# Optimization experiments

Measured on AMD Instinct MI355X. Metric: run time of the kernel, lower is better.

The kernel has to match this reference:

```python
import jax, jax.numpy as jnp
import numpy as np


def mesa_head(xh, yh, qh, lam):
    # xh = per-head 'inputs' (v_proj output), yh = 'targets' (k_proj output),
    # qh = queries; all [T, d]. lam is this head's scalar lambda.
    T, d = xh.shape
    init_inv = jnp.eye(d, dtype=xh.dtype) * lam

    def step(inv, tok):
        x_t, q_t = tok
        Hx = inv @ x_t                      # [d]   (cur_inverse @ x)
        xH = x_t @ inv                      # [d]   (x^T @ cur_inverse)
        denom = 1.0 + x_t @ Hx              # scalar: forward=1 + x^T H x
        new_inv = inv - jnp.outer(Hx, xH) / denom   # Sherman-Morrison rank-1 update
        return new_inv, new_inv @ q_t       # pred_t = S_t @ q_t

    _, preds = jax.lax.scan(step, init_inv, (xh, qh))  # preds: [T, d]

    # scaled_dot_product_attention(preds, xh, yh) with masked=True,
    # use_softmax=False, normalization=False: tril-masked linear attention.
    logits = preds @ xh.T                               # [T, T]
    mask = jnp.tril(jnp.ones((T, T), dtype=bool))
    logits = jnp.where(mask, logits, jnp.zeros((), dtype=logits.dtype))
    return logits @ yh                                  # [T, d]


def reference(x, Wq, Wk, Wv, Wo, lambdas):
    B, T, E = x.shape
    H = lambdas.shape[0]
    d = Wq.shape[1] // H
    q = (x @ Wq).reshape(B, T, H, d)   # query_heads
    k = (x @ Wk).reshape(B, T, H, d)   # target_heads
    v = (x @ Wv).reshape(B, T, H, d)   # input_heads
    # Original call: mesa(input_heads, target_heads, query_heads, lambdas, norm)
    over_batch = jax.vmap(mesa_head, in_axes=(0, 0, 0, None))
    over_heads = jax.vmap(over_batch, in_axes=(2, 2, 2, 0), out_axes=-1)
    mesa_out = over_heads(v, k, q, lambdas)             # [B, T, d, H]
    # Faithful to original: reshape combines (d, H) in that order before o_proj.
    out = mesa_out.reshape(B, T, H * d) @ Wo            # [B, T, E]
    return out


def setup_inputs() -> dict:
    key = jax.random.key(0)
    ks = jax.random.split(key, 6)
    B, T, E, H, d = 2, 1024, 512, 8, 64
    s_in = 1.0 / np.sqrt(E).astype(np.float32)
    s_out = 1.0 / np.sqrt(H * d).astype(np.float32)
    return {
        "x": jax.random.normal(ks[0], (B, T, E), dtype=jnp.float32),
        "Wq": jax.random.normal(ks[1], (E, H * d), dtype=jnp.float32) * s_in,
        "Wk": jax.random.normal(ks[2], (E, H * d), dtype=jnp.float32) * s_in,
        "Wv": jax.random.normal(ks[3], (E, H * d), dtype=jnp.float32) * s_in,
        "Wo": jax.random.normal(ks[4], (H * d, E), dtype=jnp.float32) * s_out,
        "lambdas": jnp.ones((H,), dtype=jnp.float32),
    }
```

## Files before the change

### kernel.cpp

```cpp
#include <hip/hip_runtime.h>

#define T_SEQ 1024
#define DH 64
#define NH 8
#define NB 2
#define EMB 512
#define CS 32
#define NCH 32
#define ACH 16
#define NCHAIN 16

typedef __attribute__((ext_vector_type(8))) short bf16x8;
typedef __attribute__((ext_vector_type(4))) float f32x4;

__device__ __forceinline__ int swz4(int r, int c4) {
    return r * 16 + ((c4 ^ (r >> 2)) & 15);
}

__device__ __forceinline__ void fma4(float4& o, float s, const float4& b) {
    o.x += s * b.x; o.y += s * b.y; o.z += s * b.z; o.w += s * b.w;
}

__device__ __forceinline__ ushort f2bf(float f) {
    unsigned u = __float_as_uint(f);
    return (ushort)((u + 0x7FFFu + ((u >> 16) & 1u)) >> 16);
}
__device__ __forceinline__ float bf2f(ushort h) {
    return __uint_as_float(((unsigned)h) << 16);
}
__device__ __forceinline__ void split2(float f, ushort& hi, ushort& lo) {
    hi = f2bf(f);
    lo = f2bf(f - bf2f(hi));
}

__global__ __launch_bounds__(256) void prep_qkv(
    const float* __restrict__ x, const float* __restrict__ W0,
    const float* __restrict__ W1, const float* __restrict__ W2,
    ushort* __restrict__ x_hi, ushort* __restrict__ x_lo,
    ushort* __restrict__ Wt_hi, ushort* __restrict__ Wt_lo) {
    int zz = blockIdx.z;
    int t = threadIdx.x;
    __shared__ float T[64][65];
    if (zz < 3) {
        const float* W = (zz == 0) ? W0 : (zz == 1) ? W1 : W2;
        ushort* hi = Wt_hi + (size_t)zz * 262144;
        ushort* lo = Wt_lo + (size_t)zz * 262144;
        int kk0 = blockIdx.x * 64, n0 = blockIdx.y * 64;
#pragma unroll
        for (int i = 0; i < 4; ++i) {
            int rl = i * 16 + (t >> 4);
            float4 vv = *(const float4*)&W[(size_t)(kk0 + rl) * 512 + n0 + (t & 15) * 4];
            T[rl][(t & 15) * 4 + 0] = vv.x;
            T[rl][(t & 15) * 4 + 1] = vv.y;
            T[rl][(t & 15) * 4 + 2] = vv.z;
            T[rl][(t & 15) * 4 + 3] = vv.w;
        }
        __syncthreads();
        int nl = t >> 2, kl = (t & 3) * 16;
#pragma unroll
        for (int j4 = 0; j4 < 4; ++j4) {
            ushort4 h4, l4;
            split2(T[kl + j4 * 4 + 0][nl], h4.x, l4.x);
            split2(T[kl + j4 * 4 + 1][nl], h4.y, l4.y);
            split2(T[kl + j4 * 4 + 2][nl], h4.z, l4.z);
            split2(T[kl + j4 * 4 + 3][nl], h4.w, l4.w);
            size_t dst = (size_t)(n0 + nl) * 512 + kk0 + kl + j4 * 4;
            *(ushort4*)&hi[dst] = h4;
            *(ushort4*)&lo[dst] = l4;
        }
    } else {
        int bid = blockIdx.y * 8 + blockIdx.x;
        const float4* in = (const float4*)x;
        ushort4* hi = (ushort4*)x_hi;
        ushort4* lo = (ushort4*)x_lo;
#pragma unroll
        for (int i = 0; i < 16; ++i) {
            int id = (bid * 16 + i) * 256 + t;
            float4 xv = in[id];
            ushort4 h, l;
            split2(xv.x, h.x, l.x);
            split2(xv.y, h.y, l.y);
            split2(xv.z, h.z, l.z);
            split2(xv.w, h.w, l.w);
            hi[id] = h;
            lo[id] = l;
        }
    }
}

template <int MODE>
__global__ __launch_bounds__(256) void mfma_gemm(
    const ushort* __restrict__ Ahi, const ushort* __restrict__ Alo,
    const ushort* __restrict__ Bth, const ushort* __restrict__ Btl,
    float* __restrict__ o0, float* __restrict__ o1, float* __restrict__ o2) {
    int bm = blockIdx.x, bn = blockIdx.y, zz = blockIdx.z;
    const ushort* Bh = Bth + (size_t)zz * 262144;
    const ushort* Bl = Btl + (size_t)zz * 262144;
    float* out = (MODE == 0) ? ((zz == 0) ? o0 : (zz == 1) ? o1 : o2) : o0;

    __shared__ ushort Ash[128 * 40];
    __shared__ ushort Asl[128 * 40];
    __shared__ ushort Bsh[64 * 40];
    __shared__ ushort Bsl[64 * 40];

    int tid = threadIdx.x;
    int lane = tid & 63, wid = tid >> 6;
    int wm = wid >> 1, wn = wid & 1;
    int fr = lane & 15, fk = (lane >> 4) * 8;
    int sr = tid >> 2, sc = (tid & 3) * 8;

    f32x4 zero = {0.f, 0.f, 0.f, 0.f};
    f32x4 acc[4][2];
#pragma unroll
    for (int f = 0; f < 4; ++f)
#pragma unroll
        for (int g = 0; g < 2; ++g) acc[f][g] = zero;

    const ushort* gAh = Ahi + (size_t)(bm * 128 + sr) * 512 + sc;
    const ushort* gAl = Alo + (size_t)(bm * 128 + sr) * 512 + sc;
    const ushort* gBh = Bh + (size_t)(bn * 64 + sr) * 512 + sc;
    const ushort* gBl = Bl + (size_t)(bn * 64 + sr) * 512 + sc;

    for (int k0 = 0; k0 < 512; k0 += 32) {
        uint4 a0 = *(const uint4*)(gAh + k0);
        uint4 a1 = *(const uint4*)(gAh + 64 * 512 + k0);
        uint4 a2 = *(const uint4*)(gAl + k0);
        uint4 a3 = *(const uint4*)(gAl + 64 * 512 + k0);
        uint4 b0 = *(const uint4*)(gBh + k0);
        uint4 b1 = *(const uint4*)(gBl + k0);
        __syncthreads();
        *(uint4*)&Ash[sr * 40 + sc] = a0;
        *(uint4*)&Ash[(sr + 64) * 40 + sc] = a1;
        *(uint4*)&Asl[sr * 40 + sc] = a2;
        *(uint4*)&Asl[(sr + 64) * 40 + sc] = a3;
        *(uint4*)&Bsh[sr * 40 + sc] = b0;
        *(uint4*)&Bsl[sr * 40 + sc] = b1;
        __syncthreads();
        bf16x8 ah[4], al[4], bh[2], blo[2];
#pragma unroll
        for (int f = 0; f < 4; ++f) {
            int r = wm * 64 + f * 16 + fr;
            ah[f] = *(const bf16x8*)&Ash[r * 40 + fk];
            al[f] = *(const bf16x8*)&Asl[r * 40 + fk];
        }
#pragma unroll
        for (int g = 0; g < 2; ++g) {
            int r = wn * 32 + g * 16 + fr;
            bh[g] = *(const bf16x8*)&Bsh[r * 40 + fk];
            blo[g] = *(const bf16x8*)&Bsl[r * 40 + fk];
        }
#pragma unroll
        for (int f = 0; f < 4; ++f)
#pragma unroll
            for (int g = 0; g < 2; ++g) {
                acc[f][g] = __builtin_amdgcn_mfma_f32_16x16x32_bf16(
                    ah[f], bh[g], acc[f][g], 0, 0, 0);
                acc[f][g] = __builtin_amdgcn_mfma_f32_16x16x32_bf16(
                    ah[f], blo[g], acc[f][g], 0, 0, 0);
                acc[f][g] = __builtin_amdgcn_mfma_f32_16x16x32_bf16(
                    al[f], bh[g], acc[f][g], 0, 0, 0);
            }
    }

    int rbase = (lane >> 4) * 4;
#pragma unroll
    for (int f = 0; f < 4; ++f)
#pragma unroll
        for (int g = 0; g < 2; ++g)
#pragma unroll
            for (int j = 0; j < 4; ++j) {
                int m = bm * 128 + wm * 64 + f * 16 + rbase + j;
                int n = bn * 64 + wn * 32 + g * 16 + (lane & 15);
                float val = acc[f][g][j];
                if (MODE == 0) {
                    int b = m >> 10, tt = m & 1023;
                    int h = n >> 6, d = n & 63;
                    out[(((size_t)(b * 8 + h) * 1024 + tt) << 6) + d] = val;
                } else {
                    out[(size_t)m * 512 + n] = val;
                }
            }
}

__global__ __launch_bounds__(256) void gram_kernel(
    const float* __restrict__ v, float* __restrict__ g) {
    int chain = blockIdx.x, chunk = blockIdx.y;
    const float* X = v + ((size_t)chain * T_SEQ + chunk * CS) * DH;
    __shared__ float Xs[CS * 64];
    int tid = threadIdx.x;
#pragma unroll
    for (int i = 0; i < (CS * 16) / 256; ++i)
        ((float4*)Xs)[i * 256 + tid] = ((const float4*)X)[i * 256 + tid];
    __syncthreads();

    int tx = tid & 15, ty = tid >> 4;
    float acc[4][4];
#pragma unroll
    for (int i = 0; i < 4; ++i)
#pragma unroll
        for (int j = 0; j < 4; ++j) acc[i][j] = 0.f;

#pragma unroll 4
    for (int t = 0; t < CS; ++t) {
        float a_[4], b_[4];
#pragma unroll
        for (int i = 0; i < 4; ++i) a_[i] = Xs[t * 64 + ty * 4 + i];
#pragma unroll
        for (int j = 0; j < 4; ++j) b_[j] = Xs[t * 64 + tx * 4 + j];
#pragma unroll
        for (int i = 0; i < 4; ++i)
#pragma unroll
            for (int j = 0; j < 4; ++j) acc[i][j] += a_[i] * b_[j];
    }

    float* gp = g + ((size_t)chain * NCH + chunk) * 4096;
#pragma unroll
    for (int i = 0; i < 4; ++i)
        *(float4*)(gp + (ty * 4 + i) * 64 + tx * 4) =
            make_float4(acc[i][0], acc[i][1], acc[i][2], acc[i][3]);
}

__global__ __launch_bounds__(256) void prefix_kernel(float* __restrict__ g) {
    int gid = blockIdx.x * 256 + threadIdx.x;
    int chain = gid >> 12, elem = gid & 4095;
    float* p = g + (size_t)chain * NCH * 4096 + elem;
    float vals[NCH];
#pragma unroll
    for (int c = 0; c < NCH; ++c) vals[c] = p[(size_t)c * 4096];
    float run = 0.f;
#pragma unroll
    for (int c = 0; c < NCH; ++c) {
        float t = vals[c];
        vals[c] = run;
        run += t;
    }
#pragma unroll
    for (int c = 0; c < NCH; ++c) p[(size_t)c * 4096] = vals[c];
}

__global__ __launch_bounds__(256) void invscan_kv(
    int nInv,
    const float* __restrict__ g, const float* __restrict__ v,
    const float* __restrict__ q, const float* __restrict__ lambdas,
    float* __restrict__ preds,
    const float* __restrict__ Kv, float* __restrict__ D) {
    __shared__ float smem[8192];
    int bid = blockIdx.x;
    int tid = threadIdx.x;

    if (bid < nInv) {
        int chain = bid >> 5, chunk = bid & 31;
        int row = tid >> 2, ch = tid & 3, wav = tid >> 6;
        float lam = lambdas[chain & (NH - 1)];

        float* Xs = smem;
        float* Qs = smem + 2048;
        float* Po = smem + 4096;
        float* rbufB = smem + 6144;
        float* sbufB = smem + 6272;
        float* red = smem + 6400;

        float m[16];
        {
            const float4* gp = (const float4*)(g + ((size_t)chain * NCH + chunk) * 4096);
#pragma unroll
            for (int i = 0; i < 4; ++i) {
                float4 t4 = gp[row * 16 + ch * 4 + i];
                m[i * 4 + 0] = t4.x; m[i * 4 + 1] = t4.y;
                m[i * 4 + 2] = t4.z; m[i * 4 + 3] = t4.w;
            }
        }
#pragma unroll
        for (int i = 0; i < 16; ++i)
            if (ch * 16 + i == row) m[i] += lam;

        const float4* vb = (const float4*)(v + ((size_t)chain * T_SEQ + chunk * CS) * DH);
        const float4* qb = (const float4*)(q + ((size_t)chain * T_SEQ + chunk * CS) * DH);
        ((float4*)Xs)[tid] = vb[tid];
        ((float4*)Xs)[256 + tid] = vb[256 + tid];
        ((float4*)Qs)[tid] = qb[tid];
        ((float4*)Qs)[256 + tid] = qb[256 + tid];

        if (row == 0) {
#pragma unroll
            for (int i = 0; i < 4; ++i)
                ((float4*)rbufB)[ch * 4 + i] =
                    make_float4(m[i * 4], m[i * 4 + 1], m[i * 4 + 2], m[i * 4 + 3]);
        }
        if (row == 1) {
#pragma unroll
            for (int i = 0; i < 4; ++i)
                ((float4*)sbufB)[ch * 4 + i] =
                    make_float4(m[i * 4], m[i * 4 + 1], m[i * 4 + 2], m[i * 4 + 3]);
        }
        __syncthreads();

#pragma unroll
        for (int pp = 0; pp < 32; ++pp) {
            const int p = 2 * pp;
            const float* rb = rbufB + (pp & 1) * 64;
            const float* sb = sbufB + (pp & 1) * 64;
            float r_[16], s_[16];
#pragma unroll
            for (int i = 0; i < 4; ++i) {
                float4 t4 = ((const float4*)rb)[ch * 4 + i];
                r_[i * 4] = t4.x; r_[i * 4 + 1] = t4.y;
                r_[i * 4 + 2] = t4.z; r_[i * 4 + 3] = t4.w;
                float4 u4 = ((const float4*)sb)[ch * 4 + i];
                s_[i * 4] = u4.x; s_[i * 4 + 1] = u4.y;
                s_[i * 4 + 2] = u4.z; s_[i * 4 + 3] = u4.w;
            }
            float rp = rb[p], rp2 = rb[p + 1], sp2 = sb[p + 1];
            float gr = rb[row], gs = sb[row];
            float i1 = 1.f / rp;
            float al = rp2 * i1;
            float i2 = 1.f / (sp2 - al * rp2);
            float c0, ca, cb;
            if (row == p) {
                c0 = 0.f; ca = i1 + al * al * i2; cb = -al * i2;
            } else if (row == p + 1) {
                c0 = 0.f; ca = -al * i2; cb = i2;
            } else {
                float b2 = (gs - al * gr) * i2;
                c0 = 1.f; ca = al * b2 - gr * i1; cb = -b2;
            }
#pragma unroll
            for (int i = 0; i < 16; ++i) m[i] = c0 * m[i] + ca * r_[i] + cb * s_[i];
            if (ch == (p >> 4)) {
                m[p & 15] = -ca;
                m[(p & 15) + 1] = -cb;
            }
            if (pp < 31) {
                if (row == p + 2) {
#pragma unroll
                    for (int i = 0; i < 4; ++i)
                        ((float4*)(rbufB + ((pp + 1) & 1) * 64))[ch * 4 + i] =
                            make_float4(m[i * 4], m[i * 4 + 1], m[i * 4 + 2], m[i * 4 + 3]);
                }
                if (row == p + 3) {
#pragma unroll
                    for (int i = 0; i < 4; ++i)
                        ((float4*)(sbufB + ((pp + 1) & 1) * 64))[ch * 4 + i] =
                            make_float4(m[i * 4], m[i * 4 + 1], m[i * 4 + 2], m[i * 4 + 3]);
                }
            }
            __syncthreads();
        }

#pragma unroll
        for (int tp = 0; tp < 16; ++tp) {
            const int ta = 2 * tp, tb2 = 2 * tp + 1;
            const int par = tp & 1;
            float pu = 0.f, pw = 0.f, pza = 0.f, pzb = 0.f;
#pragma unroll
            for (int i = 0; i < 4; ++i) {
                float4 xa = ((const float4*)(Xs + ta * 64))[ch * 4 + i];
                float4 xb = ((const float4*)(Xs + tb2 * 64))[ch * 4 + i];
                float4 qa = ((const float4*)(Qs + ta * 64))[ch * 4 + i];
                float4 q4 = ((const float4*)(Qs + tb2 * 64))[ch * 4 + i];
                pu += m[i * 4] * xa.x + m[i * 4 + 1] * xa.y + m[i * 4 + 2] * xa.z + m[i * 4 + 3] * xa.w;
                pw += m[i * 4] * xb.x + m[i * 4 + 1] * xb.y + m[i * 4 + 2] * xb.z + m[i * 4 + 3] * xb.w;
                pza += m[i * 4] * qa.x + m[i * 4 + 1] * qa.y + m[i * 4 + 2] * qa.z + m[i * 4 + 3] * qa.w;
                pzb += m[i * 4] * q4.x + m[i * 4 + 1] * q4.y + m[i * 4 + 2] * q4.z + m[i * 4 + 3] * q4.w;
            }
            pu += __shfl_xor(pu, 1); pu += __shfl_xor(pu, 2);
            pw += __shfl_xor(pw, 1); pw += __shfl_xor(pw, 2);
            pza += __shfl_xor(pza, 1); pza += __shfl_xor(pza, 2);
            pzb += __shfl_xor(pzb, 1); pzb += __shfl_xor(pzb, 2);
            float u = -pu, w = -pw, za = -pza, zb = -pzb;
            float* rbufP = rbufB + par * 64;
            float* sbufP = sbufB + par * 64;
            if (ch == 0) rbufP[row] = u;
            if (ch == 1) sbufP[row] = w;
            float a_ = Xs[ta * 64 + row], b_ = Xs[tb2 * 64 + row];
            float qa_ = Qs[ta * 64 + row], qb_ = Qs[tb2 * 64 + row];
            float d0 = a_ * u, d1 = b_ * u, d2 = b_ * w;
            float d3 = qa_ * u, d4 = qb_ * u, d5 = qb_ * w;
#pragma unroll
            for (int off = 32; off; off >>= 1) {
                d0 += __shfl_xor(d0, off); d1 += __shfl_xor(d1, off);
                d2 += __shfl_xor(d2, off); d3 += __shfl_xor(d3, off);
                d4 += __shfl_xor(d4, off); d5 += __shfl_xor(d5, off);
            }
            if ((tid & 63) == 0) {
                red[par * 24 + 0 * 4 + wav] = d0; red[par * 24 + 1 * 4 + wav] = d1;
                red[par * 24 + 2 * 4 + wav] = d2; red[par * 24 + 3 * 4 + wav] = d3;
                red[par * 24 + 4 * 4 + wav] = d4; red[par * 24 + 5 * 4 + wav] = d5;
            }
            __syncthreads();
            const float* rp_ = red + par * 24;
            float saa = 0.25f * (rp_[0] + rp_[1] + rp_[2] + rp_[3]);
            float sab = 0.25f * (rp_[4] + rp_[5] + rp_[6] + rp_[7]);
            float sbb = 0.25f * (rp_[8] + rp_[9] + rp_[10] + rp_[11]);
            float c1  = 0.25f * (rp_[12] + rp_[13] + rp_[14] + rp_[15]);
            float c2  = 0.25f * (rp_[16] + rp_[17] + rp_[18] + rp_[19]);
            float c3  = 0.25f * (rp_[20] + rp_[21] + rp_[22] + rp_[23]);
            float k1 = 1.f / (1.f + saa);
            float al2 = sab * k1;
            float k2 = 1.f / (1.f + sbb - sab * al2);
            float vr = w - al2 * u;
            if (ch == 0) Po[ta * 64 + row] = za - (c1 * k1) * u;
            if (ch == 1) Po[tb2 * 64 + row] = zb - (c2 * k1) * u - (k2 * (c3 - al2 * c2)) * vr;
            float cu = k1 * u - al2 * k2 * vr;
            float cw = k2 * vr;
#pragma unroll
            for (int i = 0; i < 4; ++i) {
                float4 uj = ((const float4*)rbufP)[ch * 4 + i];
                float4 wj = ((const float4*)sbufP)[ch * 4 + i];
                m[i * 4 + 0] += cu * uj.x + cw * wj.x;
                m[i * 4 + 1] += cu * uj.y + cw * wj.y;
                m[i * 4 + 2] += cu * uj.z + cw * wj.z;
                m[i * 4 + 3] += cu * uj.w + cw * wj.w;
            }
        }
        __syncthreads();

        float4* po4 = (float4*)(preds + ((size_t)chain * T_SEQ + chunk * CS) * DH);
        po4[tid] = ((const float4*)Po)[tid];
        po4[256 + tid] = ((const float4*)Po)[256 + tid];
    } else {
        int kb = bid - nInv;
        int chain = kb >> 4, ck = kb & 15;
        float* Vs = smem;
        float* Ks2 = smem + 4096;
        const float4* Vb = (const float4*)(v + ((size_t)chain * T_SEQ + ck * 64) * DH);
        const float4* Kb = (const float4*)(Kv + ((size_t)chain * T_SEQ + ck * 64) * DH);
#pragma unroll
        for (int i = 0; i < 4; ++i) {
            ((float4*)Vs)[i * 256 + tid] = Vb[i * 256 + tid];
            ((float4*)Ks2)[i * 256 + tid] = Kb[i * 256 + tid];
        }
        __syncthreads();

        int tx = tid & 15, ty = tid >> 4;
        float acc[4][4];
#pragma unroll
        for (int i = 0; i < 4; ++i)
#pragma unroll
            for (int j = 0; j < 4; ++j) acc[i][j] = 0.f;

#pragma unroll 4
        for (int t = 0; t < 64; ++t) {
            float a_[4], b_[4];
#pragma unroll
            for (int i = 0; i < 4; ++i) a_[i] = Vs[t * 64 + ty * 4 + i];
#pragma unroll
            for (int j = 0; j < 4; ++j) b_[j] = Ks2[t * 64 + tx * 4 + j];
#pragma unroll
            for (int i = 0; i < 4; ++i)
#pragma unroll
                for (int j = 0; j < 4; ++j) acc[i][j] += a_[i] * b_[j];
        }

        float* dp = D + ((size_t)chain * ACH + ck) * 4096;
#pragma unroll
        for (int i = 0; i < 4; ++i)
            *(float4*)(dp + (ty * 4 + i) * 64 + tx * 4) =
                make_float4(acc[i][0], acc[i][1], acc[i][2], acc[i][3]);
    }
}

__global__ __launch_bounds__(256) void kv_prefix(float* __restrict__ d) {
    int gid = blockIdx.x * 256 + threadIdx.x;
    int chain = gid >> 12, elem = gid & 4095;
    float* p = d + (size_t)chain * ACH * 4096 + elem;
    float vals[ACH];
#pragma unroll
    for (int c = 0; c < ACH; ++c) vals[c] = p[(size_t)c * 4096];
    float run = 0.f;
#pragma unroll
    for (int c = 0; c < ACH; ++c) {
        float t = vals[c];
        vals[c] = run;
        run += t;
    }
#pragma unroll
    for (int c = 0; c < ACH; ++c) p[(size_t)c * 4096] = vals[c];
}

__global__ __launch_bounds__(256) void attn_wot(
    const float* __restrict__ P, const float* __restrict__ V,
    const float* __restrict__ Kv, const float* __restrict__ C,
    ushort* __restrict__ A2_hi, ushort* __restrict__ A2_lo,
    const float* __restrict__ Wo,
    ushort* __restrict__ Wot_hi, ushort* __restrict__ Wot_lo) {
    __shared__ float4 smem4[3072];
    int bid = blockIdx.x;
    int tid = threadIdx.x;

    if (bid < 256) {
        int ck = bid & 15, bh = bid >> 4;
        int tx = tid & 15, ty = tid >> 4;
        float4* Ps = smem4;
        float4* Bs = smem4 + 1024;
        float4* Ks = smem4 + 2048;

        int lr = tid >> 2, lc = tid & 3;
        const float4* Pb = (const float4*)(P + ((size_t)bh * T_SEQ + ck * 64) * DH);
        const float4* Vb = (const float4*)(V + ((size_t)bh * T_SEQ + ck * 64) * DH);
        const float4* Kb = (const float4*)(Kv + ((size_t)bh * T_SEQ + ck * 64) * DH);
        const float4* Cb = (const float4*)(C + ((size_t)bh * ACH + ck) * 4096);
#pragma unroll
        for (int i = 0; i < 4; ++i) {
            Ps[swz4(lr, lc + i * 4)] = Pb[lr * 16 + lc + i * 4];
            Bs[swz4(lr, lc + i * 4)] = Cb[lr * 16 + lc + i * 4];
            Ks[swz4(lr, lc + i * 4)] = Kb[lr * 16 + lc + i * 4];
        }

        float4 o[4];
        o[0] = o[1] = o[2] = o[3] = make_float4(0.f, 0.f, 0.f, 0.f);
        __syncthreads();

        const float* Pf = (const float*)Ps;
#pragma unroll 4
        for (int j = 0; j < 64; ++j) {
            float4 b4 = Bs[swz4(j, tx)];
#pragma unroll
            for (int i = 0; i < 4; ++i) {
                float s = Pf[swz4(ty * 4 + i, j >> 2) * 4 + (j & 3)];
                fma4(o[i], s, b4);
            }
        }
        __syncthreads();

#pragma unroll
        for (int i = 0; i < 4; ++i)
            Bs[swz4(lr, lc + i * 4)] = Vb[lr * 16 + lc + i * 4];
        __syncthreads();

        float4 sa[4][4];
#pragma unroll
        for (int i = 0; i < 4; ++i)
#pragma unroll
            for (int j = 0; j < 4; ++j) sa[i][j] = make_float4(0.f, 0.f, 0.f, 0.f);
#pragma unroll
        for (int d4 = 0; d4 < 16; ++d4) {
            float4 a[4], b[4];
#pragma unroll
            for (int i = 0; i < 4; ++i) a[i] = Ps[swz4(ty * 4 + i, d4)];
#pragma unroll
            for (int j = 0; j < 4; ++j) b[j] = Bs[swz4(tx * 4 + j, d4)];
#pragma unroll
            for (int i = 0; i < 4; ++i)
#pragma unroll
                for (int j = 0; j < 4; ++j) {
                    sa[i][j].x += a[i].x * b[j].x;
                    sa[i][j].y += a[i].y * b[j].y;
                    sa[i][j].z += a[i].z * b[j].z;
                    sa[i][j].w += a[i].w * b[j].w;
                }
        }
        __syncthreads();

#pragma unroll
        for (int i = 0; i < 4; ++i) {
            int m = ty * 4 + i;
            float sv[4];
#pragma unroll
            for (int j = 0; j < 4; ++j) {
                float s = sa[i][j].x + sa[i][j].y + sa[i][j].z + sa[i][j].w;
                if ((tx * 4 + j) > m) s = 0.f;
                sv[j] = s;
            }
            Bs[swz4(m, tx)] = make_float4(sv[0], sv[1], sv[2], sv[3]);
        }
        __syncthreads();

        const float* Sf = (const float*)Bs;
#pragma unroll 4
        for (int j = 0; j < 64; ++j) {
            float4 b4 = Ks[swz4(j, tx)];
#pragma unroll
            for (int i = 0; i < 4; ++i) {
                float s = Sf[swz4(ty * 4 + i, j >> 2) * 4 + (j & 3)];
                fma4(o[i], s, b4);
            }
        }

        int kkb = ((bh & 7) << 6) + tx * 4;
#pragma unroll
        for (int i = 0; i < 4; ++i) {
            int t = ck * 64 + ty * 4 + i;
            size_t mrow = (size_t)((bh >> 3) << 10) + t;
            ushort4 h, l;
            split2(o[i].x, h.x, l.x);
            split2(o[i].y, h.y, l.y);
            split2(o[i].z, h.z, l.z);
            split2(o[i].w, h.w, l.w);
            *(ushort4*)&A2_hi[mrow * 512 + kkb] = h;
            *(ushort4*)&A2_lo[mrow * 512 + kkb] = l;
        }
    } else {
        float* Tf = (float*)smem4;
        int wb = bid - 256;
        int kk0 = (wb >> 3) * 64, n0 = (wb & 7) * 64;
#pragma unroll
        for (int i = 0; i < 4; ++i) {
            int rl = i * 16 + (tid >> 4);
            int rs = rl * 8 + (kk0 >> 6);
            float4 vv = *(const float4*)&Wo[(size_t)rs * 512 + n0 + (tid & 15) * 4];
            Tf[rl * 65 + (tid & 15) * 4 + 0] = vv.x;
            Tf[rl * 65 + (tid & 15) * 4 + 1] = vv.y;
            Tf[rl * 65 + (tid & 15) * 4 + 2] = vv.z;
            Tf[rl * 65 + (tid & 15) * 4 + 3] = vv.w;
        }
        __syncthreads();
        int nl = tid >> 2, kl = (tid & 3) * 16;
#pragma unroll
        for (int j4 = 0; j4 < 4; ++j4) {
            ushort4 h4, l4;
            split2(Tf[(kl + j4 * 4 + 0) * 65 + nl], h4.x, l4.x);
            split2(Tf[(kl + j4 * 4 + 1) * 65 + nl], h4.y, l4.y);
            split2(Tf[(kl + j4 * 4 + 2) * 65 + nl], h4.z, l4.z);
            split2(Tf[(kl + j4 * 4 + 3) * 65 + nl], h4.w, l4.w);
            size_t dst = (size_t)(n0 + nl) * 512 + kk0 + kl + j4 * 4;
            *(ushort4*)&Wot_hi[dst] = h4;
            *(ushort4*)&Wot_lo[dst] = l4;
        }
    }
}

extern "C" void kernel_launch(void* const* d_in, const int* in_sizes, int n_in,
                              void* d_out, int out_size, void* d_ws, size_t ws_size,
                              hipStream_t stream) {
    const float* x = (const float*)d_in[0];
    const float* Wq = (const float*)d_in[1];
    const float* Wk = (const float*)d_in[2];
    const float* Wv = (const float*)d_in[3];
    const float* Wo = (const float*)d_in[4];
    const float* lambdas = (const float*)d_in[5];
    float* out = (float*)d_out;

    float* ws = (float*)d_ws;
    const size_t SZ = (size_t)NB * NH * T_SEQ * DH;
    float* q = ws;
    float* k = ws + SZ;
    float* v = ws + 2 * SZ;
    float* preds = ws + 3 * SZ;
    ushort* x_hi = (ushort*)(ws + 3 * SZ);
    ushort* x_lo = (ushort*)(ws + 3 * SZ + SZ / 2);
    float* g = ws + 4 * SZ;
    ushort* Wt_hi = (ushort*)(ws + 4 * SZ);
    ushort* Wt_lo = (ushort*)(ws + 4 * SZ + 393216);
    ushort* A2_hi = (ushort*)(ws + 5 * SZ);
    ushort* A2_lo = (ushort*)(ws + 5 * SZ + SZ / 2);
    ushort* Wot_hi = (ushort*)ws;
    ushort* Wot_lo = (ushort*)(ws + 131072);

    bool big = ws_size >= (size_t)7 * SZ * sizeof(float);
    float* dbuf = big ? (ws + 6 * SZ) : g;

    prep_qkv<<<dim3(8, 8, 4), 256, 0, stream>>>(x, Wq, Wk, Wv,
                                                x_hi, x_lo, Wt_hi, Wt_lo);
    mfma_gemm<0><<<dim3(16, 8, 3), 256, 0, stream>>>(
        x_hi, x_lo, Wt_hi, Wt_lo, q, k, v);
    gram_kernel<<<dim3(NCHAIN, NCH), 256, 0, stream>>>(v, g);
    prefix_kernel<<<dim3(256), 256, 0, stream>>>(g);
    if (big) {
        invscan_kv<<<dim3(NCHAIN * NCH + NCHAIN * ACH), 256, 0, stream>>>(
            NCHAIN * NCH, g, v, q, lambdas, preds, k, dbuf);
    } else {
        invscan_kv<<<dim3(NCHAIN * NCH), 256, 0, stream>>>(
            NCHAIN * NCH, g, v, q, lambdas, preds, k, dbuf);
        invscan_kv<<<dim3(NCHAIN * ACH), 256, 0, stream>>>(
            0, g, v, q, lambdas, preds, k, dbuf);
    }
    kv_prefix<<<dim3(256), 256, 0, stream>>>(dbuf);
    attn_wot<<<dim3(320), 256, 0, stream>>>(preds, v, k, dbuf, A2_hi, A2_lo,
                                            Wo, Wot_hi, Wot_lo);
    mfma_gemm<1><<<dim3(16, 8, 1), 256, 0, stream>>>(
        (const ushort*)A2_hi, (const ushort*)A2_lo, Wot_hi, Wot_lo,
        out, out, out);
}
```

Measured before the change: 123.7 us.

## Process four pivots per step in in-kernel matrix inversion to halve barriers

The Gauss-Jordan style in-place inversion now eliminates four pivot rows per iteration instead of two. Each thread updates the two extra pivot rows locally to finish the second 2x2 block, so the loop runs 16 barrier-separated steps instead of 32. The shared row buffer grows to hold four rows per parity. The trade-off is extra register pressure and arithmetic per step, plus a larger shared buffer, in exchange for fewer __syncthreads and fewer shared-memory round trips.

```diff
diff --git a/kernel.cpp b/kernel.cpp
--- a/kernel.cpp
+++ b/kernel.cpp
@@ -256,9 +256,8 @@
         float* Xs = smem;
         float* Qs = smem + 2048;
         float* Po = smem + 4096;
-        float* rbufB = smem + 6144;
-        float* sbufB = smem + 6272;
-        float* red = smem + 6400;
+        float* Rq = smem + 6144;
+        float* red = smem + 6656;
 
         float m[16];
         {
@@ -281,40 +280,47 @@
         ((float4*)Qs)[tid] = qb[tid];
         ((float4*)Qs)[256 + tid] = qb[256 + tid];
 
-        if (row == 0) {
+        if (row < 4) {
 #pragma unroll
             for (int i = 0; i < 4; ++i)
-                ((float4*)rbufB)[ch * 4 + i] =
+                ((float4*)(Rq + row * 64))[ch * 4 + i] =
                     make_float4(m[i * 4], m[i * 4 + 1], m[i * 4 + 2], m[i * 4 + 3]);
         }
-        if (row == 1) {
-#pragma unroll
-            for (int i = 0; i < 4; ++i)
-                ((float4*)sbufB)[ch * 4 + i] =
-                    make_float4(m[i * 4], m[i * 4 + 1], m[i * 4 + 2], m[i * 4 + 3]);
-        }
-        __syncthreads();
-
-#pragma unroll
-        for (int pp = 0; pp < 32; ++pp) {
-            const int p = 2 * pp;
-            const float* rb = rbufB + (pp & 1) * 64;
-            const float* sb = sbufB + (pp & 1) * 64;
-            float r_[16], s_[16];
+        __syncthreads();
+
+#pragma unroll
+        for (int pp = 0; pp < 16; ++pp) {
+            const int p = 4 * pp;
+            const float* rb = Rq + (pp & 1) * 256;
+            const float* sb = rb + 64;
+            const float* tb = rb + 128;
+            const float* ub = rb + 192;
+            float r_[16], s_[16], t_[16], u_[16];
 #pragma unroll
             for (int i = 0; i < 4; ++i) {
-                float4 t4 = ((const float4*)rb)[ch * 4 + i];
-                r_[i * 4] = t4.x; r_[i * 4 + 1] = t4.y;
-                r_[i * 4 + 2] = t4.z; r_[i * 4 + 3] = t4.w;
-                float4 u4 = ((const float4*)sb)[ch * 4 + i];
-                s_[i * 4] = u4.x; s_[i * 4 + 1] = u4.y;
-                s_[i * 4 + 2] = u4.z; s_[i * 4 + 3] = u4.w;
-            }
-            float rp = rb[p], rp2 = rb[p + 1], sp2 = sb[p + 1];
+                float4 a4 = ((const float4*)rb)[ch * 4 + i];
+                r_[i * 4] = a4.x; r_[i * 4 + 1] = a4.y; r_[i * 4 + 2] = a4.z; r_[i * 4 + 3] = a4.w;
+                float4 b4 = ((const float4*)sb)[ch * 4 + i];
+                s_[i * 4] = b4.x; s_[i * 4 + 1] = b4.y; s_[i * 4 + 2] = b4.z; s_[i * 4 + 3] = b4.w;
+                float4 c4 = ((const float4*)tb)[ch * 4 + i];
+                t_[i * 4] = c4.x; t_[i * 4 + 1] = c4.y; t_[i * 4 + 2] = c4.z; t_[i * 4 + 3] = c4.w;
+                float4 d4 = ((const float4*)ub)[ch * 4 + i];
+                u_[i * 4] = d4.x; u_[i * 4 + 1] = d4.y; u_[i * 4 + 2] = d4.z; u_[i * 4 + 3] = d4.w;
+            }
+            float rp = rb[p], rp1 = rb[p + 1], sp1 = sb[p + 1];
+            float rT = rb[p + 2], sT = sb[p + 2];
+            float rU = rb[p + 3], sU = sb[p + 3];
+            float tp2 = tb[p + 2], tp3 = tb[p + 3], up3 = ub[p + 3];
             float gr = rb[row], gs = sb[row];
+            float tr = tb[row], ur = ub[row];
+
             float i1 = 1.f / rp;
-            float al = rp2 * i1;
-            float i2 = 1.f / (sp2 - al * rp2);
+            float al = rp1 * i1;
+            float i2 = 1.f / (sp1 - al * rp1);
+            float b2T = (sT - al * rT) * i2;
+            float caT = al * b2T - rT * i1, cbT = -b2T;
+            float b2U = (sU - al * rU) * i2;
+            float caU = al * b2U - rU * i1, cbU = -b2U;
             float c0, ca, cb;
             if (row == p) {
                 c0 = 0.f; ca = i1 + al * al * i2; cb = -al * i2;
@@ -325,22 +331,65 @@
                 c0 = 1.f; ca = al * b2 - gr * i1; cb = -b2;
             }
 #pragma unroll
-            for (int i = 0; i < 16; ++i) m[i] = c0 * m[i] + ca * r_[i] + cb * s_[i];
-            if (ch == (p >> 4)) {
-                m[p & 15] = -ca;
-                m[(p & 15) + 1] = -cb;
-            }
-            if (pp < 31) {
-                if (row == p + 2) {
+            for (int i = 0; i < 16; ++i) {
+                float upd = c0 * m[i] + ca * r_[i] + cb * s_[i];
+                int col = ch * 16 + i;
+                upd = (col == p) ? -ca : upd;
+                upd = (col == p + 1) ? -cb : upd;
+                m[i] = upd;
+            }
+#pragma unroll
+            for (int i = 0; i < 16; ++i) {
+                float tv = t_[i] + caT * r_[i] + cbT * s_[i];
+                float uv = u_[i] + caU * r_[i] + cbU * s_[i];
+                int col = ch * 16 + i;
+                tv = (col == p) ? -caT : tv;
+                tv = (col == p + 1) ? -cbT : tv;
+                uv = (col == p) ? -caU : uv;
+                uv = (col == p + 1) ? -cbU : uv;
+                t_[i] = tv;
+                u_[i] = uv;
+            }
+
+            float rpB = tp2 + caT * rT + cbT * sT;
+            float rp3B = tp3 + caT * rU + cbT * sU;
+            float sp3B = up3 + caU * rU + cbU * sU;
+            float grB, gsB;
+            if (row == p) {
+                grB = -caT; gsB = -caU;
+            } else if (row == p + 1) {
+                grB = -cbT; gsB = -cbU;
+            } else {
+                grB = tr + caT * gr + cbT * gs;
+                gsB = ur + caU * gr + cbU * gs;
+            }
+            float i1B = 1.f / rpB;
+            float alB = rp3B * i1B;
+            float i2B = 1.f / (sp3B - alB * rp3B);
+            float c0B, cc, cd;
+            if (row == p + 2) {
+                c0B = 0.f; cc = i1B + alB * alB * i2B; cd = -alB * i2B;
+            } else if (row == p + 3) {
+                c0B = 0.f; cc = -alB * i2B; cd = i2B;
+            } else {
+                float b2B = (gsB - alB * grB) * i2B;
+                c0B = 1.f; cc = alB * b2B - grB * i1B; cd = -b2B;
+            }
+#pragma unroll
+            for (int i = 0; i < 16; ++i) {
+                float upd = c0B * m[i] + cc * t_[i] + cd * u_[i];
+                int col = ch * 16 + i;
+                upd = (col == p + 2) ? -cc : upd;
+                upd = (col == p + 3) ? -cd : upd;
+                m[i] = upd;
+            }
+
+            if (pp < 15) {
+                if (row >= p + 4 && row < p + 8) {
+                    float* dst = Rq + ((pp + 1) & 1) * 256 + (row - (p + 4)) * 64;
 #pragma unroll
                     for (int i = 0; i < 4; ++i)
-                        ((float4*)(rbufB + ((pp + 1) & 1) * 64))[ch * 4 + i] =
-                            make_float4(m[i * 4], m[i * 4 + 1], m[i * 4 + 2], m[i * 4 + 3]);
-                }
-                if (row == p + 3) {
-#pragma unroll
-                    for (int i = 0; i < 4; ++i)
-                        ((float4*)(sbufB + ((pp + 1) & 1) * 64))[ch * 4 + i] =
+                        ((float4*)dst)[ch * 4 + i] =
                             make_float4(m[i * 4], m[i * 4 + 1], m[i * 4 + 2], m[i * 4 + 3]);
                 }
             }
@@ -368,8 +417,8 @@
             pza += __shfl_xor(pza, 1); pza += __shfl_xor(pza, 2);
             pzb += __shfl_xor(pzb, 1); pzb += __shfl_xor(pzb, 2);
             float u = -pu, w = -pw, za = -pza, zb = -pzb;
-            float* rbufP = rbufB + par * 64;
-            float* sbufP = sbufB + par * 64;
+            float* rbufP = Rq + par * 256;
+            float* sbufP = Rq + par * 256 + 64;
             if (ch == 0) rbufP[row] = u;
             if (ch == 1) sbufP[row] = w;
             float a_ = Xs[ta * 64 + row], b_ = Xs[tb2 * 64 + row];
```

After: 123.2 us. No clear change (-0.4%).
